# Kernel optimization log

Hardware: AMD Instinct MI355X
Metric: run time of the kernel (lower is better)

## Reference

```python
import jax, jax.numpy as jnp
import numpy as np

# KWConv2d config: in=256, out=256, k=3, s=1, p=1, groups=1, bias=False
# warehouse: 32 spatial cells of shape [64, 64, 3, 3]; num_fourier_basis=0; temp_value=0
B, CIN, H, W_ = 32, 256, 56, 56
OUT = 256
NUM_CELLS, CO, CI, KH, KW = 32, 64, 64, 3, 3
HIDDEN = 16                 # max(int(256 * 0.0625), 16)
GO, GI, GS = OUT // CO, CIN // CI, 1
M = GO * GI * GS            # num_local_mixture = 16
P = NUM_CELLS + 1           # kw_planes_per_mixture = 33
KWP = P * M                 # kw_planes = 528


def setup_inputs() -> dict:
    key = jax.random.key(0)
    ks = jax.random.split(key, 4)
    s = 0.02
    return {
        "x": jax.random.normal(ks[0], (B, CIN, H, W_), jnp.float32),
        "cells": jax.random.normal(ks[1], (NUM_CELLS, CO, CI, KH, KW), jnp.float32) * s,
        "fc1_w": jax.random.normal(ks[2], (HIDDEN, CIN), jnp.float32) * s,
        "fc1_b": jnp.zeros((HIDDEN,), jnp.float32),
        "ln_g": jnp.ones((HIDDEN,), jnp.float32),
        "ln_b": jnp.zeros((HIDDEN,), jnp.float32),
        "sp_w": jax.random.normal(ks[3], (KWP, HIDDEN), jnp.float32) * s,
        "sp_b": jnp.zeros((KWP,), jnp.float32),
    }


def _attention(x, fc1_w, fc1_b, ln_g, ln_b, sp_w, sp_b):
    # AdaptiveAvgPool1d(1) over flattened spatial dims == global mean
    pooled = x.mean(axis=(2, 3))                      # [B, CIN]
    h = pooled @ fc1_w.T + fc1_b                      # [B, HIDDEN]
    mu = h.mean(-1, keepdims=True)
    var = ((h - mu) ** 2).mean(-1, keepdims=True)
    h = (h - mu) * jax.lax.rsqrt(var + 1e-5) * ln_g + ln_b
    h = jax.nn.relu(h)
    a = h @ sp_w.T + sp_b                             # spatial_head -> [B, KWP]
    a = a.reshape(-1, P)                              # [B*M, P]
    a = a / (jnp.abs(a).sum(axis=1, keepdims=True) + 0.001)  # L1 normalize per mixture
    # temp_value = 0 -> attention unchanged; drop last (zero) column
    return a[:, :-1]                                  # [B*M, NUM_CELLS]


def reference(x, cells, fc1_w, fc1_b, ln_g, ln_b, sp_w, sp_b):
    att = _attention(x, fc1_w, fc1_b, ln_g, ln_b, sp_w, sp_b)  # [B*M, NUM_CELLS]
    w = cells.reshape(NUM_CELLS, -1)                  # [NUM_CELLS, CO*CI*KH*KW]
    agg = att @ w                                     # [B*M, CO*CI*KH*KW]
    agg = agg.reshape(B, GS, GO, GI, CO, CI, KH, KW)
    agg = agg.transpose(0, 2, 4, 3, 5, 1, 6, 7)       # torch permute (0,2,4,3,5,1,6,7)
    agg = agg.reshape(B * OUT, CIN, KH, KW)           # per-sample kernels (groups=1)
    # grouped-conv trick: fold batch into channels, groups = B
    xr = x.reshape(1, B * CIN, H, W_)
    out = jax.lax.conv_general_dilated(
        xr, agg, window_strides=(1, 1), padding=((1, 1), (1, 1)),
        dimension_numbers=("NCHW", "OIHW", "NCHW"), feature_group_count=B)
    return out.reshape(B, OUT, H, W_)
```

## Files before the change

### kernel.cpp

```cpp
#include <hip/hip_runtime.h>
#include <stdint.h>

typedef unsigned short ush;
typedef __bf16   bf16x8 __attribute__((ext_vector_type(8)));
typedef float    f32x4  __attribute__((ext_vector_type(4)));
typedef uint32_t u32x4  __attribute__((ext_vector_type(4)));

union U16B { u32x4 u; bf16x8 b; };
union P8   { ush us[8]; u32x4 v; };

template<int V> struct ICx { static constexpr int value = V; };

__device__ __forceinline__ ush f2bf(float f) {
    union { float f; uint32_t u; } v; v.f = f;
    uint32_t r = v.u + 0x7FFFu + ((v.u >> 16) & 1u);
    return (ush)(r >> 16);
}

#define HWPX  3136
#define POOL_OFF   58720256UL
#define ATT_OFF    58753024UL
#define WAGG_OFF   58818560UL

__global__ void k_halo(u32x4* __restrict__ xT16, u32x4* __restrict__ pooled16) {
    int i = blockIdx.x * 256 + threadIdx.x;
    int rl = i >> 3, s = i & 7;
    u32x4 z = (u32x4)(0u);
    size_t byte = (size_t)rl * 4096 + (s < 4 ? s * 16 : 3648 + (s - 4) * 16);
    xT16[byte >> 4] = z;
    if (blockIdx.x < 8) pooled16[blockIdx.x * 256 + threadIdx.x] = z;
}

__global__ void k_transpose(const float* __restrict__ x, ush* __restrict__ xT,
                            float* __restrict__ pooled) {
    __shared__ float tile[64][65];
    int blk = blockIdx.x;
    int b   = blk / 196;
    int rem = blk % 196;
    int icg = rem / 49;
    int pxg = rem % 49;
    int t = threadIdx.x;

    {
        int icl  = t >> 2, part = t & 3;
        const float* src = x + (size_t)(b * 256 + icg * 64 + icl) * HWPX + pxg * 64 + part * 16;
        #pragma unroll
        for (int k = 0; k < 4; ++k) {
            f32x4 v = *(const f32x4*)(src + k * 4);
            tile[icl][part * 16 + k * 4 + 0] = v[0];
            tile[icl][part * 16 + k * 4 + 1] = v[1];
            tile[icl][part * 16 + k * 4 + 2] = v[2];
            tile[icl][part * 16 + k * 4 + 3] = v[3];
        }
    }
    __syncthreads();

    if (t < 64) {
        float s = 0.f;
        #pragma unroll 8
        for (int p = 0; p < 64; ++p) s += tile[t][p];
        atomicAdd(pooled + b * 256 + icg * 64 + t, s);
    }

    {
        int pxl = t >> 2, icq = t & 3;
        int px  = pxg * 64 + pxl;
        int row = px / 56;
        int col = px - row * 56;
        int p   = col + 1;
        int xorp = (p & 3) ^ ((p >> 2) & 3);
        int icg32   = icg * 2 + (icq >> 1);
        int subbase = (icq & 1) * 2;
        P8 lo, hi;
        #pragma unroll
        for (int m = 0; m < 8; ++m) {
            lo.us[m] = f2bf(tile[icq * 16 + m][pxl]);
            hi.us[m] = f2bf(tile[icq * 16 + 8 + m][pxl]);
        }
        size_t base = (((size_t)(b * 8 + icg32) * 56 + row) * 64 + p) * 32;
        *(u32x4*)(xT + base + (size_t)((subbase ^ xorp) * 8))       = lo.v;
        *(u32x4*)(xT + base + (size_t)(((subbase + 1) ^ xorp) * 8)) = hi.v;
    }
}

__global__ void k_attn(const float* __restrict__ pooled,
                       const float* __restrict__ fc1_w, const float* __restrict__ fc1_b,
                       const float* __restrict__ ln_g,  const float* __restrict__ ln_b,
                       const float* __restrict__ sp_w,  const float* __restrict__ sp_b,
                       float* __restrict__ att) {
    __shared__ float hs[32][16];
    int t = threadIdx.x;
    {
        int b = t >> 4, j = t & 15;
        float acc = 0.f;
        for (int c = 0; c < 256; ++c) acc += pooled[b * 256 + c] * fc1_w[j * 256 + c];
        hs[b][j] = fc1_b[j] + acc * (1.0f / 3136.0f);
    }
    __syncthreads();
    if (t < 32) {
        float mu = 0.f;
        #pragma unroll
        for (int j = 0; j < 16; ++j) mu += hs[t][j];
        mu *= (1.0f / 16.0f);
        float var = 0.f;
        #pragma unroll
        for (int j = 0; j < 16; ++j) { float d = hs[t][j] - mu; var += d * d; }
        var *= (1.0f / 16.0f);
        float inv = rsqrtf(var + 1e-5f);
        #pragma unroll
        for (int j = 0; j < 16; ++j) {
            float v = (hs[t][j] - mu) * inv * ln_g[j] + ln_b[j];
            hs[t][j] = fmaxf(v, 0.f);
        }
    }
    __syncthreads();
    {
        int b = t >> 4, m = t & 15;
        float a[33];
        #pragma unroll 1
        for (int i = 0; i < 33; ++i) {
            int p = m * 33 + i;
            float acc = sp_b[p];
            #pragma unroll
            for (int j = 0; j < 16; ++j) acc += hs[b][j] * sp_w[p * 16 + j];
            a[i] = acc;
        }
        float s = 0.f;
        #pragma unroll
        for (int i = 0; i < 33; ++i) s += fabsf(a[i]);
        float inv = 1.0f / (s + 0.001f);
        #pragma unroll
        for (int c = 0; c < 32; ++c) att[(b * 16 + m) * 32 + c] = a[c] * inv;
    }
}

__global__ void k_agg(const float* __restrict__ cells, const float* __restrict__ att,
                      ush* __restrict__ wagg) {
    __shared__ float at[512];
    int blk = blockIdx.x;
    int b = blk >> 6, co = blk & 63;
    int t = threadIdx.x;
    for (int i = t; i < 512; i += 256) at[i] = att[b * 512 + i];
    __syncthreads();
    int ci = t & 63, gi = t >> 6;
    float acc[4][9];
    #pragma unroll
    for (int g = 0; g < 4; ++g)
        #pragma unroll
        for (int k = 0; k < 9; ++k) acc[g][k] = 0.f;
    for (int c = 0; c < 32; ++c) {
        float a0 = at[(0 + gi) * 32 + c];
        float a1 = at[(4 + gi) * 32 + c];
        float a2 = at[(8 + gi) * 32 + c];
        float a3 = at[(12 + gi) * 32 + c];
        const float* cp = cells + (size_t)c * 36864 + co * 576 + ci * 9;
        #pragma unroll
        for (int k = 0; k < 9; ++k) {
            float cv = cp[k];
            acc[0][k] += a0 * cv; acc[1][k] += a1 * cv;
            acc[2][k] += a2 * cv; acc[3][k] += a3 * cv;
        }
    }
    #pragma unroll
    for (int g = 0; g < 4; ++g)
        #pragma unroll
        for (int k = 0; k < 9; ++k)
            wagg[((size_t)(b * 9 + k) * 256 + g * 64 + co) * 256 + gi * 64 + ci] = f2bf(acc[g][k]);
}

__global__ __launch_bounds__(256, 3) void k_conv(const ush* __restrict__ xT,
                                                 const ush* __restrict__ wagg,
                                                 float* __restrict__ out) {
    __shared__ __align__(16) ush xs[2][12288];

    int tid = threadIdx.x;
    int wg  = blockIdx.x;
    int xcd = wg & 7;
    int kk  = wg >> 3;
    int gq  = kk / 14;
    int sp  = kk - gq * 14;
    int g   = gq * 8 + xcd;
    int b   = g >> 2, octile = g & 3;
    int row0 = sp * 4, oc0 = octile * 64;

    int lane = tid & 63, w = tid >> 6;
    int wm = w >> 1, wn = w & 1;
    int l15 = lane & 15, s4 = lane >> 4;

    {
        u32x4 z = (u32x4)(0u);
        #pragma unroll
        for (int i = 0; i < 12; ++i) ((u32x4*)xs)[tid + i * 256] = z;
    }

    int prow[7], pq[7];
    #pragma unroll
    for (int j = 0; j < 7; ++j) {
        int px = wn * 112 + j * 16 + l15;
        prow[j] = px / 56;
        pq[j]   = px - prow[j] * 56;
    }

    unsigned vmask = 0;
    #pragma unroll
    for (int k = 0; k < 6; ++k) {
        int grow = row0 - 1 + k;
        if (grow >= 0 && grow < 56) vmask |= 1u << k;
    }

    const ush* wb = wagg + (size_t)b * 9 * 65536 + (size_t)(oc0 + wm * 32 + l15) * 256 + s4 * 8;
    const ush* xb = xT + (size_t)b * 8 * 56 * 2048 + (size_t)tid * 8;

    f32x4 acc[2][7];
    #pragma unroll
    for (int mi = 0; mi < 2; ++mi)
        #pragma unroll
        for (int j = 0; j < 7; ++j) acc[mi][j] = (f32x4)(0.f);

    U16B wp0a, wp0b, wp1a, wp1b;
    wp0a.u = *(const u32x4*)(wb);
    wp0b.u = *(const u32x4*)(wb + 4096);
    wp1a.u = *(const u32x4*)(wb + 65536);
    wp1b.u = *(const u32x4*)(wb + 65536 + 4096);

    __syncthreads();

    {
        u32x4 ld[6];
        #pragma unroll
        for (int k = 0; k < 6; ++k)
            if (vmask & (1u << k)) ld[k] = *(const u32x4*)(xb + (size_t)(row0 - 1 + k) * 2048);
        #pragma unroll
        for (int k = 0; k < 6; ++k)
            if (vmask & (1u << k)) *(u32x4*)(&xs[0][k * 2048 + tid * 8]) = ld[k];
    }
    __syncthreads();

    auto chunk_body = [&](auto parc, int chunk) {
        constexpr int PAR = decltype(parc)::value;
        u32x4 ld[6];
        bool pre = chunk < 7;
        if (pre) {
            #pragma unroll
            for (int k = 0; k < 6; ++k)
                if (vmask & (1u << k))
                    ld[k] = *(const u32x4*)(xb + (size_t)((chunk + 1) * 56 + row0 - 1 + k) * 2048);
        }
        const ush* xsb = xs[PAR];
        #pragma unroll
        for (int tap = 0; tap < 9; ++tap) {
            const int dy = tap / 3, dx = tap % 3;
            U16B a0, a1;
            if ((PAR + tap) & 1) { a0 = wp1a; a1 = wp1b; } else { a0 = wp0a; a1 = wp0b; }
            {
                int nt = tap + 2, nc = chunk;
                if (nt >= 9) { nt -= 9; ++nc; }
                if (nc < 8) {
                    const ush* wnx = wb + (size_t)nt * 65536 + (size_t)nc * 32;
                    if ((PAR + tap) & 1) {
                        wp1a.u = *(const u32x4*)(wnx);
                        wp1b.u = *(const u32x4*)(wnx + 4096);
                    } else {
                        wp0a.u = *(const u32x4*)(wnx);
                        wp0b.u = *(const u32x4*)(wnx + 4096);
                    }
                }
            }
            #pragma unroll
            for (int j = 0; j < 7; ++j) {
                int q    = pq[j] + dx;
                int slot = s4 ^ (q & 3) ^ ((q >> 2) & 3);
                int off  = ((prow[j] + dy) * 64 + q) * 32 + slot * 8;
                U16B bj; bj.u = *(const u32x4*)(xsb + off);
                acc[0][j] = __builtin_amdgcn_mfma_f32_16x16x32_bf16(bj.b, a0.b, acc[0][j], 0, 0, 0);
                acc[1][j] = __builtin_amdgcn_mfma_f32_16x16x32_bf16(bj.b, a1.b, acc[1][j], 0, 0, 0);
            }
        }
        if (pre) {
            ush* xn = xs[PAR ^ 1];
            #pragma unroll
            for (int k = 0; k < 6; ++k)
                if (vmask & (1u << k)) *(u32x4*)(&xn[k * 2048 + tid * 8]) = ld[k];
        }
        __syncthreads();
    };

    for (int c2 = 0; c2 < 8; c2 += 2) {
        chunk_body(ICx<0>{}, c2);
        chunk_body(ICx<1>{}, c2 + 1);
    }

    int pxbase = row0 * 56 + wn * 112 + s4 * 4;
    #pragma unroll
    for (int mi = 0; mi < 2; ++mi) {
        int oc = oc0 + wm * 32 + mi * 16 + l15;
        float* o = out + (size_t)(b * 256 + oc) * HWPX + pxbase;
        #pragma unroll
        for (int j = 0; j < 7; ++j)
            *(f32x4*)(o + j * 16) = acc[mi][j];
    }
}

extern "C" void kernel_launch(void* const* d_in, const int* in_sizes, int n_in,
                              void* d_out, int out_size, void* d_ws, size_t ws_size,
                              hipStream_t stream) {
    const float* x     = (const float*)d_in[0];
    const float* cells = (const float*)d_in[1];
    const float* fc1_w = (const float*)d_in[2];
    const float* fc1_b = (const float*)d_in[3];
    const float* ln_g  = (const float*)d_in[4];
    const float* ln_b  = (const float*)d_in[5];
    const float* sp_w  = (const float*)d_in[6];
    const float* sp_b  = (const float*)d_in[7];
    float* out = (float*)d_out;

    char* ws = (char*)d_ws;
    ush*   xT     = (ush*)ws;
    float* pooled = (float*)(ws + POOL_OFF);
    float* att    = (float*)(ws + ATT_OFF);
    ush*   wagg   = (ush*)(ws + WAGG_OFF);

    k_halo<<<448, 256, 0, stream>>>((u32x4*)ws, (u32x4*)pooled);
    k_transpose<<<6272, 256, 0, stream>>>(x, xT, pooled);
    k_attn<<<1, 512, 0, stream>>>(pooled, fc1_w, fc1_b, ln_g, ln_b, sp_w, sp_b, att);
    k_agg<<<2048, 256, 0, stream>>>(cells, att, wagg);
    k_conv<<<1792, 256, 0, stream>>>(xT, wagg, out);
}
```

Before: 287.8 us.

## Double conv output-channel tile and stream input rows via direct global-to-LDS loads

The conv kernel now covers 128 output channels per workgroup instead of 64. Each wave keeps 4x7 accumulators, so every LDS input fragment feeds four MFMAs and the input tile is staged half as often, with half as many workgroups. The input prefetch into LDS now uses global_load_lds instead of register staging, and the LDS swizzle is simplified to match the new write pattern. In exchange, register pressure rises (launch bounds drop to 2 blocks per CU), and there are fewer blocks to hide latency behind.

```diff
diff --git a/kernel.cpp b/kernel.cpp
--- a/kernel.cpp
+++ b/kernel.cpp
@@ -15,6 +15,12 @@
     union { float f; uint32_t u; } v; v.f = f;
     uint32_t r = v.u + 0x7FFFu + ((v.u >> 16) & 1u);
     return (ush)(r >> 16);
+}
+
+__device__ __forceinline__ void gl_lds16(const ush* g, ush* l) {
+    __builtin_amdgcn_global_load_lds(
+        (const __attribute__((address_space(1))) uint32_t*)g,
+        (__attribute__((address_space(3))) uint32_t*)l, 16, 0, 0);
 }
 
 #define HWPX  3136
@@ -68,7 +74,7 @@
         int row = px / 56;
         int col = px - row * 56;
         int p   = col + 1;
-        int xorp = (p & 3) ^ ((p >> 2) & 3);
+        int xorp = (p >> 1) & 3;
         int icg32   = icg * 2 + (icq >> 1);
         int subbase = (icq & 1) * 2;
         P8 lo, hi;
@@ -168,7 +174,7 @@
             wagg[((size_t)(b * 9 + k) * 256 + g * 64 + co) * 256 + gi * 64 + ci] = f2bf(acc[g][k]);
 }
 
-__global__ __launch_bounds__(256, 3) void k_conv(const ush* __restrict__ xT,
+__global__ __launch_bounds__(256, 2) void k_conv(const ush* __restrict__ xT,
                                                  const ush* __restrict__ wagg,
                                                  float* __restrict__ out) {
     __shared__ __align__(16) ush xs[2][12288];
@@ -180,8 +186,8 @@
     int gq  = kk / 14;
     int sp  = kk - gq * 14;
     int g   = gq * 8 + xcd;
-    int b   = g >> 2, octile = g & 3;
-    int row0 = sp * 4, oc0 = octile * 64;
+    int b   = g >> 1, octile = g & 1;
+    int row0 = sp * 4, oc0 = octile * 128;
 
     int lane = tid & 63, w = tid >> 6;
     int wm = w >> 1, wn = w & 1;
@@ -208,79 +214,72 @@
         if (grow >= 0 && grow < 56) vmask |= 1u << k;
     }
 
-    const ush* wb = wagg + (size_t)b * 9 * 65536 + (size_t)(oc0 + wm * 32 + l15) * 256 + s4 * 8;
+    const ush* wb = wagg + (size_t)b * 9 * 65536 + (size_t)(oc0 + wm * 64 + l15) * 256 + s4 * 8;
     const ush* xb = xT + (size_t)b * 8 * 56 * 2048 + (size_t)tid * 8;
-
-    f32x4 acc[2][7];
-    #pragma unroll
-    for (int mi = 0; mi < 2; ++mi)
+    ush* lq = &xs[0][0];
+
+    f32x4 acc[4][7];
+    #pragma unroll
+    for (int mi = 0; mi < 4; ++mi)
         #pragma unroll
         for (int j = 0; j < 7; ++j) acc[mi][j] = (f32x4)(0.f);
 
-    U16B wp0a, wp0b, wp1a, wp1b;
-    wp0a.u = *(const u32x4*)(wb);
-    wp0b.u = *(const u32x4*)(wb + 4096);
-    wp1a.u = *(const u32x4*)(wb + 65536);
-    wp1b.u = *(const u32x4*)(wb + 65536 + 4096);
-
-    __syncthreads();
-
-    {
-        u32x4 ld[6];
-        #pragma unroll
-        for (int k = 0; k < 6; ++k)
-            if (vmask & (1u << k)) ld[k] = *(const u32x4*)(xb + (size_t)(row0 - 1 + k) * 2048);
-        #pragma unroll
-        for (int k = 0; k < 6; ++k)
-            if (vmask & (1u << k)) *(u32x4*)(&xs[0][k * 2048 + tid * 8]) = ld[k];
-    }
+    U16B wpa[2][4];
+    #pragma unroll
+    for (int mi = 0; mi < 4; ++mi) {
+        wpa[0][mi].u = *(const u32x4*)(wb + mi * 4096);
+        wpa[1][mi].u = *(const u32x4*)(wb + 65536 + mi * 4096);
+    }
+
+    __syncthreads();
+
+    #pragma unroll
+    for (int k = 0; k < 6; ++k)
+        if (vmask & (1u << k))
+            gl_lds16(xb + (size_t)(row0 - 1 + k) * 2048, lq + k * 2048 + w * 512);
     __syncthreads();
 
     auto chunk_body = [&](auto parc, int chunk) {
         constexpr int PAR = decltype(parc)::value;
-        u32x4 ld[6];
-        bool pre = chunk < 7;
-        if (pre) {
+        if (chunk < 7) {
             #pragma unroll
             for (int k = 0; k < 6; ++k)
                 if (vmask & (1u << k))
-                    ld[k] = *(const u32x4*)(xb + (size_t)((chunk + 1) * 56 + row0 - 1 + k) * 2048);
+                    gl_lds16(xb + (size_t)((chunk + 1) * 56 + row0 - 1 + k) * 2048,
+                             lq + (PAR ^ 1) * 12288 + k * 2048 + w * 512);
         }
         const ush* xsb = xs[PAR];
         #pragma unroll
         for (int tap = 0; tap < 9; ++tap) {
             const int dy = tap / 3, dx = tap % 3;
-            U16B a0, a1;
-            if ((PAR + tap) & 1) { a0 = wp1a; a1 = wp1b; } else { a0 = wp0a; a1 = wp0b; }
+            U16B a0, a1, a2, a3;
+            if ((PAR + tap) & 1) { a0 = wpa[1][0]; a1 = wpa[1][1]; a2 = wpa[1][2]; a3 = wpa[1][3]; }
+            else                 { a0 = wpa[0][0]; a1 = wpa[0][1]; a2 = wpa[0][2]; a3 = wpa[0][3]; }
             {
                 int nt = tap + 2, nc = chunk;
                 if (nt >= 9) { nt -= 9; ++nc; }
                 if (nc < 8) {
                     const ush* wnx = wb + (size_t)nt * 65536 + (size_t)nc * 32;
                     if ((PAR + tap) & 1) {
-                        wp1a.u = *(const u32x4*)(wnx);
-                        wp1b.u = *(const u32x4*)(wnx + 4096);
+                        #pragma unroll
+                        for (int mi = 0; mi < 4; ++mi) wpa[1][mi].u = *(const u32x4*)(wnx + mi * 4096);
                     } else {
-                        wp0a.u = *(const u32x4*)(wnx);
-                        wp0b.u = *(const u32x4*)(wnx + 4096);
+                        #pragma unroll
+                        for (int mi = 0; mi < 4; ++mi) wpa[0][mi].u = *(const u32x4*)(wnx + mi * 4096);
                     }
                 }
             }
             #pragma unroll
             for (int j = 0; j < 7; ++j) {
                 int q    = pq[j] + dx;
-                int slot = s4 ^ (q & 3) ^ ((q >> 2) & 3);
+                int slot = s4 ^ ((q >> 1) & 3);
                 int off  = ((prow[j] + dy) * 64 + q) * 32 + slot * 8;
                 U16B bj; bj.u = *(const u32x4*)(xsb + off);
                 acc[0][j] = __builtin_amdgcn_mfma_f32_16x16x32_bf16(bj.b, a0.b, acc[0][j], 0, 0, 0);
                 acc[1][j] = __builtin_amdgcn_mfma_f32_16x16x32_bf16(bj.b, a1.b, acc[1][j], 0, 0, 0);
+                acc[2][j] = __builtin_amdgcn_mfma_f32_16x16x32_bf16(bj.b, a2.b, acc[2][j], 0, 0, 0);
+                acc[3][j] = __builtin_amdgcn_mfma_f32_16x16x32_bf16(bj.b, a3.b, acc[3][j], 0, 0, 0);
             }
-        }
-        if (pre) {
-            ush* xn = xs[PAR ^ 1];
-            #pragma unroll
-            for (int k = 0; k < 6; ++k)
-                if (vmask & (1u << k)) *(u32x4*)(&xn[k * 2048 + tid * 8]) = ld[k];
         }
         __syncthreads();
     };
@@ -292,8 +291,8 @@
 
     int pxbase = row0 * 56 + wn * 112 + s4 * 4;
     #pragma unroll
-    for (int mi = 0; mi < 2; ++mi) {
-        int oc = oc0 + wm * 32 + mi * 16 + l15;
+    for (int mi = 0; mi < 4; ++mi) {
+        int oc = oc0 + wm * 64 + mi * 16 + l15;
         float* o = out + (size_t)(b * 256 + oc) * HWPX + pxbase;
         #pragma unroll
         for (int j = 0; j < 7; ++j)
@@ -324,5 +323,5 @@
     k_transpose<<<6272, 256, 0, stream>>>(x, xT, pooled);
     k_attn<<<1, 512, 0, stream>>>(pooled, fc1_w, fc1_b, ln_g, ln_b, sp_w, sp_b, att);
     k_agg<<<2048, 256, 0, stream>>>(cells, att, wagg);
-    k_conv<<<1792, 256, 0, stream>>>(xT, wagg, out);
-}
+    k_conv<<<896, 256, 0, stream>>>(xT, wagg, out);
+}
```

New measurement: 275.8 us. 4.2% less time.
